# Performance work log

Measured on AMD Instinct MI355X. Metric: run time of the kernel, lower is better.

## Reference

```python
import jax, jax.numpy as jnp
import numpy as np

N = 200000
IN_F = 512
OUT_F = 256
NEG_INF = -9e15


def setup_inputs() -> dict:
    key = jax.random.key(0)
    k1, k2, k3, k4 = jax.random.split(key, 4)
    inp = jax.random.normal(k1, (N, IN_F), dtype=jnp.float32)
    adj = jax.random.randint(k2, (N, OUT_F), 0, 2, dtype=jnp.int32)
    # xavier_uniform with gain=1.414
    g = 1.414
    bW = g * np.sqrt(6.0 / (IN_F + OUT_F))
    W = jax.random.uniform(k3, (IN_F, OUT_F), jnp.float32, -bW, bW)
    ba = g * np.sqrt(6.0 / (2 * OUT_F + 1))
    a = jax.random.uniform(k4, (2 * OUT_F, 1), jnp.float32, -ba, ba)
    return {"input": inp, "adj": adj, "W": W, "a": a}


def reference(input, adj, W, a):
    h = input @ W                      # [N, M]
    M = h.shape[1]
    # a_input[n,m,:] = concat(h[n], h[n]) for every m, so
    # (a_input @ a)[n,m] = h[n] . (a[:M] + a[M:]) — constant over m.
    s = h @ (a[:M, 0] + a[M:, 0])      # [N]
    e = jax.nn.leaky_relu(s, negative_slope=0.2)[:, None]  # [N, 1]
    e = jnp.broadcast_to(e, (h.shape[0], M))               # [N, M]
    masked = jnp.where(adj > 0, e, NEG_INF)
    attention = jax.nn.softmax(masked, axis=1)             # rowwise softmax
    h_prime = attention * h                                # elementwise combine
    return jax.nn.elu(h_prime)
```

## Files before the change

kernel.cpp:

```cpp
#include <hip/hip_runtime.h>
#include <hip/hip_bf16.h>
#include <math.h>


#define NROWS  200000
#define K_DIM  512
#define C_DIM  256
#define BM     128
#define BK     32
#define NCHUNK 16
#define LSTR   40
#define CHUNK_BYTES (C_DIM * LSTR * 2)
#define WPACK_BYTES (NCHUNK * CHUNK_BYTES)

typedef __bf16 bf16x8 __attribute__((ext_vector_type(8)));
typedef float  f32x4  __attribute__((ext_vector_type(4)));
typedef float  f32x16 __attribute__((ext_vector_type(16)));

__global__ void prep_w(const float* __restrict__ W,
                       __bf16* __restrict__ whi, __bf16* __restrict__ wlo) {
  int idx = blockIdx.x * 256 + threadIdx.x;
  int k = idx >> 8, c = idx & 255;
  float w = W[idx];
  __bf16 h = (__bf16)w;
  __bf16 l = (__bf16)(w - (float)h);
  int off = ((k >> 5) * C_DIM + c) * LSTR + (k & 31);
  whi[off] = h;
  wlo[off] = l;
}

__device__ __forceinline__ void gload16(const void* g, void* l) {
  __builtin_amdgcn_global_load_lds(
      (const __attribute__((address_space(1))) unsigned*)g,
      (__attribute__((address_space(3))) unsigned*)l, 16, 0, 0);
}

__global__ void __launch_bounds__(512)
gat_kernel(const float* __restrict__ X, const int* __restrict__ adj,
           const __bf16* __restrict__ whi, const __bf16* __restrict__ wlo,
           float* __restrict__ out) {
  __shared__ __bf16 Ah[2][BM * LSTR];
  __shared__ __bf16 Al[2][BM * LSTR];
  __shared__ __bf16 Bh[2][C_DIM * LSTR];
  __shared__ __bf16 Bl[2][C_DIM * LSTR];
  __shared__ float    invl[BM];
  __shared__ unsigned maskl[BM][8];

  const int tid  = threadIdx.x;
  const int lane = tid & 63;
  const int wv   = tid >> 6;
  const int wm   = wv >> 1;
  const int wn   = wv & 1;
  const int l31  = lane & 31;
  const int hi   = lane >> 5;
  const long r0  = (long)blockIdx.x * BM;

  {
    const int r = tid >> 2, q = tid & 3;
    long rr = r0 + r; if (rr > NROWS - 1) rr = NROWS - 1;
    const int4* ap = (const int4*)(adj + rr * C_DIM + q * 64);
    unsigned w0 = 0, w1 = 0; int cnt = 0;
#pragma unroll
    for (int j = 0; j < 16; ++j) {
      int4 v = ap[j];
      unsigned b = (unsigned)((v.x > 0) | ((v.y > 0) << 1) |
                              ((v.z > 0) << 2) | ((v.w > 0) << 3));
      cnt += __popc(b);
      if (j < 8) w0 |= b << (j * 4); else w1 |= b << ((j - 8) * 4);
    }
    cnt += __shfl_xor(cnt, 1);
    cnt += __shfl_xor(cnt, 2);
    if (cnt == 0) { w0 = 0xffffffffu; w1 = 0xffffffffu; }
    maskl[r][q * 2]     = w0;
    maskl[r][q * 2 + 1] = w1;
    if (q == 0) invl[r] = (cnt > 0) ? (1.0f / (float)cnt) : (1.0f / 256.0f);
  }

  const int sr = tid >> 2;
  const int sq = tid & 3;
  long srow = r0 + sr; if (srow > NROWS - 1) srow = NROWS - 1;
  const float* xbase = X + srow * K_DIM + sq * 8;
  const int aoff = sr * LSTR + sq * 8;
  const __bf16* bsrc = (wv < 4) ? whi : wlo;
  const int bwq = wv & 3;

  f32x16 acc[4];
#pragma unroll
  for (int n = 0; n < 4; ++n) acc[n] = (f32x16)(0.0f);

  f32x4 xa, xb;
  {
    xa = *(const f32x4*)(xbase + 0);
    xb = *(const f32x4*)(xbase + 4);
    const char* s = (const char*)bsrc;
    char* dh = (char*)((wv < 4) ? Bh[0] : Bl[0]);
#pragma unroll
    for (int i = 0; i < 5; ++i) {
      int off = (bwq * 5 + i) * 1024;
      gload16(s + off + lane * 16, dh + off);
    }
    bf16x8 hv, lv;
#pragma unroll
    for (int e = 0; e < 4; ++e) {
      float f0 = xa[e], f1 = xb[e];
      __bf16 h0 = (__bf16)f0, h1 = (__bf16)f1;
      hv[e] = h0; hv[e + 4] = h1;
      lv[e] = (__bf16)(f0 - (float)h0);
      lv[e + 4] = (__bf16)(f1 - (float)h1);
    }
    *(bf16x8*)&Ah[0][aoff] = hv;
    *(bf16x8*)&Al[0][aoff] = lv;
  }
  __syncthreads();

  int cur = 0;
  for (int ck = 0; ck < NCHUNK; ++ck) {
    const bool pf = (ck + 1 < NCHUNK);
    if (pf) {
      xa = *(const f32x4*)(xbase + (ck + 1) * BK);
      xb = *(const f32x4*)(xbase + (ck + 1) * BK + 4);
      const char* s = (const char*)bsrc + (ck + 1) * CHUNK_BYTES;
      char* dh = (char*)((wv < 4) ? Bh[cur ^ 1] : Bl[cur ^ 1]);
#pragma unroll
      for (int i = 0; i < 5; ++i) {
        int off = (bwq * 5 + i) * 1024;
        gload16(s + off + lane * 16, dh + off);
      }
    }
#pragma unroll
    for (int s2 = 0; s2 < 2; ++s2) {
      const int ko = s2 * 16 + hi * 8;
      bf16x8 ah = *(const bf16x8*)&Ah[cur][(wm * 32 + l31) * LSTR + ko];
      bf16x8 al = *(const bf16x8*)&Al[cur][(wm * 32 + l31) * LSTR + ko];
#pragma unroll
      for (int n = 0; n < 4; ++n) {
        const int coff = (wn * 128 + n * 32 + l31) * LSTR + ko;
        bf16x8 bh = *(const bf16x8*)&Bh[cur][coff];
        bf16x8 bl = *(const bf16x8*)&Bl[cur][coff];
        acc[n] = __builtin_amdgcn_mfma_f32_32x32x16_bf16(ah, bh, acc[n], 0, 0, 0);
        acc[n] = __builtin_amdgcn_mfma_f32_32x32x16_bf16(ah, bl, acc[n], 0, 0, 0);
        acc[n] = __builtin_amdgcn_mfma_f32_32x32x16_bf16(al, bh, acc[n], 0, 0, 0);
      }
    }
    if (pf) {
      bf16x8 hv, lv;
#pragma unroll
      for (int e = 0; e < 4; ++e) {
        float f0 = xa[e], f1 = xb[e];
        __bf16 h0 = (__bf16)f0, h1 = (__bf16)f1;
        hv[e] = h0; hv[e + 4] = h1;
        lv[e] = (__bf16)(f0 - (float)h0);
        lv[e + 4] = (__bf16)(f1 - (float)h1);
      }
      *(bf16x8*)&Ah[cur ^ 1][aoff] = hv;
      *(bf16x8*)&Al[cur ^ 1][aoff] = lv;
    }
    __syncthreads();
    cur ^= 1;
  }

#pragma unroll
  for (int n = 0; n < 4; ++n) {
    const int col = wn * 128 + n * 32 + l31;
    const int mwi = col >> 5;
#pragma unroll
    for (int g = 0; g < 4; ++g) {
#pragma unroll
      for (int rb = 0; rb < 4; ++rb) {
        const int reg = g * 4 + rb;
        const int row = wm * 32 + rb + g * 8 + hi * 4;
        const long rr = r0 + row;
        if (rr < NROWS) {
          float inv = invl[row];
          unsigned mw = maskl[row][mwi];
          float h = acc[n][reg];
          float o = 0.0f;
          if ((mw >> (col & 31)) & 1u) {
            float hp = h * inv;
            o = hp > 0.0f ? hp : expm1f(hp);
          }
          out[rr * C_DIM + col] = o;
        }
      }
    }
  }
}

extern "C" void kernel_launch(void* const* d_in, const int* in_sizes, int n_in,
                              void* d_out, int out_size, void* d_ws, size_t ws_size,
                              hipStream_t stream) {
  const float* X   = (const float*)d_in[0];
  const int*   adj = (const int*)d_in[1];
  const float* W   = (const float*)d_in[2];
  __bf16* whi = (__bf16*)d_ws;
  __bf16* wlo = (__bf16*)((char*)d_ws + WPACK_BYTES);

  prep_w<<<512, 256, 0, stream>>>(W, whi, wlo);
  const int nblk = (NROWS + BM - 1) / BM;
  gat_kernel<<<nblk, 512, 0, stream>>>(X, adj, whi, wlo, (float*)d_out);
}
```

Baseline: 869.7 us.

## Replace split-bf16 triple MFMA with single fp16 MFMA and stream adjacency mask

Drops the hi/lo bf16 splitting of X and W, which cost three MFMAs per tile, and uses a single fp16 MFMA on fp16 copies instead, halving LDS and global traffic for W. The adjacency mask load is interleaved into the K-loop prefetch so it overlaps with compute rather than sitting in a serial prologue. The trailing barrier now runs only when a prefetch happened, and launch bounds request more occupancy. This gives up some precision (fp16 has a single rounding and a limited range) in exchange for less compute and memory traffic.

Measured after the change: 888.8 us. 2.2% more time.

```diff
diff --git a/kernel.cpp b/kernel.cpp
--- a/kernel.cpp
+++ b/kernel.cpp
@@ -1,5 +1,6 @@
 #include <hip/hip_runtime.h>
 #include <hip/hip_bf16.h>
+#include <hip/hip_fp16.h>
 #include <math.h>
 
 
@@ -13,20 +14,14 @@
 #define CHUNK_BYTES (C_DIM * LSTR * 2)
 #define WPACK_BYTES (NCHUNK * CHUNK_BYTES)
 
-typedef __bf16 bf16x8 __attribute__((ext_vector_type(8)));
-typedef float  f32x4  __attribute__((ext_vector_type(4)));
-typedef float  f32x16 __attribute__((ext_vector_type(16)));
+typedef _Float16 f16x8 __attribute__((ext_vector_type(8)));
+typedef float    f32x4  __attribute__((ext_vector_type(4)));
+typedef float    f32x16 __attribute__((ext_vector_type(16)));
 
-__global__ void prep_w(const float* __restrict__ W,
-                       __bf16* __restrict__ whi, __bf16* __restrict__ wlo) {
+__global__ void prep_w(const float* __restrict__ W, _Float16* __restrict__ wh) {
   int idx = blockIdx.x * 256 + threadIdx.x;
   int k = idx >> 8, c = idx & 255;
-  float w = W[idx];
-  __bf16 h = (__bf16)w;
-  __bf16 l = (__bf16)(w - (float)h);
-  int off = ((k >> 5) * C_DIM + c) * LSTR + (k & 31);
-  whi[off] = h;
-  wlo[off] = l;
+  wh[((k >> 5) * C_DIM + c) * LSTR + (k & 31)] = (_Float16)W[idx];
 }
 
 __device__ __forceinline__ void gload16(const void* g, void* l) {
@@ -35,14 +30,11 @@
       (__attribute__((address_space(3))) unsigned*)l, 16, 0, 0);
 }
 
-__global__ void __launch_bounds__(512)
+__global__ void __launch_bounds__(512, 4)
 gat_kernel(const float* __restrict__ X, const int* __restrict__ adj,
-           const __bf16* __restrict__ whi, const __bf16* __restrict__ wlo,
-           float* __restrict__ out) {
-  __shared__ __bf16 Ah[2][BM * LSTR];
-  __shared__ __bf16 Al[2][BM * LSTR];
-  __shared__ __bf16 Bh[2][C_DIM * LSTR];
-  __shared__ __bf16 Bl[2][C_DIM * LSTR];
+           const _Float16* __restrict__ wh, float* __restrict__ out) {
+  __shared__ _Float16 Ah[2][BM * LSTR];
+  __shared__ _Float16 Bh[2][C_DIM * LSTR];
   __shared__ float    invl[BM];
   __shared__ unsigned maskl[BM][8];
 
@@ -55,109 +47,86 @@
   const int hi   = lane >> 5;
   const long r0  = (long)blockIdx.x * BM;
 
-  {
-    const int r = tid >> 2, q = tid & 3;
-    long rr = r0 + r; if (rr > NROWS - 1) rr = NROWS - 1;
-    const int4* ap = (const int4*)(adj + rr * C_DIM + q * 64);
-    unsigned w0 = 0, w1 = 0; int cnt = 0;
-#pragma unroll
-    for (int j = 0; j < 16; ++j) {
-      int4 v = ap[j];
-      unsigned b = (unsigned)((v.x > 0) | ((v.y > 0) << 1) |
-                              ((v.z > 0) << 2) | ((v.w > 0) << 3));
-      cnt += __popc(b);
-      if (j < 8) w0 |= b << (j * 4); else w1 |= b << ((j - 8) * 4);
-    }
-    cnt += __shfl_xor(cnt, 1);
-    cnt += __shfl_xor(cnt, 2);
-    if (cnt == 0) { w0 = 0xffffffffu; w1 = 0xffffffffu; }
-    maskl[r][q * 2]     = w0;
-    maskl[r][q * 2 + 1] = w1;
-    if (q == 0) invl[r] = (cnt > 0) ? (1.0f / (float)cnt) : (1.0f / 256.0f);
-  }
-
   const int sr = tid >> 2;
   const int sq = tid & 3;
   long srow = r0 + sr; if (srow > NROWS - 1) srow = NROWS - 1;
   const float* xbase = X + srow * K_DIM + sq * 8;
   const int aoff = sr * LSTR + sq * 8;
-  const __bf16* bsrc = (wv < 4) ? whi : wlo;
-  const int bwq = wv & 3;
+  const int4* adjp = (const int4*)(adj + srow * C_DIM) + sq * 16;
 
   f32x16 acc[4];
 #pragma unroll
   for (int n = 0; n < 4; ++n) acc[n] = (f32x16)(0.0f);
 
-  f32x4 xa, xb;
+  f32x4 xa, xb; int4 av;
   {
     xa = *(const f32x4*)(xbase + 0);
     xb = *(const f32x4*)(xbase + 4);
-    const char* s = (const char*)bsrc;
-    char* dh = (char*)((wv < 4) ? Bh[0] : Bl[0]);
+    av = adjp[0];
 #pragma unroll
-    for (int i = 0; i < 5; ++i) {
-      int off = (bwq * 5 + i) * 1024;
-      gload16(s + off + lane * 16, dh + off);
+    for (int i = 0; i < 3; ++i) {
+      int bi = wv + i * 8;
+      if (bi < 20)
+        gload16((const char*)wh + bi * 1024 + lane * 16, (char*)Bh[0] + bi * 1024);
     }
-    bf16x8 hv, lv;
+    f16x8 hv;
 #pragma unroll
-    for (int e = 0; e < 4; ++e) {
-      float f0 = xa[e], f1 = xb[e];
-      __bf16 h0 = (__bf16)f0, h1 = (__bf16)f1;
-      hv[e] = h0; hv[e + 4] = h1;
-      lv[e] = (__bf16)(f0 - (float)h0);
-      lv[e + 4] = (__bf16)(f1 - (float)h1);
-    }
-    *(bf16x8*)&Ah[0][aoff] = hv;
-    *(bf16x8*)&Al[0][aoff] = lv;
+    for (int e = 0; e < 4; ++e) { hv[e] = (_Float16)xa[e]; hv[e + 4] = (_Float16)xb[e]; }
+    *(f16x8*)&Ah[0][aoff] = hv;
   }
   __syncthreads();
 
+  unsigned w0 = 0, w1 = 0; int cnt = 0;
   int cur = 0;
   for (int ck = 0; ck < NCHUNK; ++ck) {
     const bool pf = (ck + 1 < NCHUNK);
+    f32x4 nxa, nxb; int4 nav;
     if (pf) {
-      xa = *(const f32x4*)(xbase + (ck + 1) * BK);
-      xb = *(const f32x4*)(xbase + (ck + 1) * BK + 4);
-      const char* s = (const char*)bsrc + (ck + 1) * CHUNK_BYTES;
-      char* dh = (char*)((wv < 4) ? Bh[cur ^ 1] : Bl[cur ^ 1]);
+      nxa = *(const f32x4*)(xbase + (ck + 1) * BK);
+      nxb = *(const f32x4*)(xbase + (ck + 1) * BK + 4);
+      nav = adjp[ck + 1];
+      const char* s = (const char*)wh + (ck + 1) * CHUNK_BYTES;
+      char* d = (char*)Bh[cur ^ 1];
 #pragma unroll
-      for (int i = 0; i < 5; ++i) {
-        int off = (bwq * 5 + i) * 1024;
-        gload16(s + off + lane * 16, dh + off);
+      for (int i = 0; i < 3; ++i) {
+        int bi = wv + i * 8;
+        if (bi < 20) gload16(s + bi * 1024 + lane * 16, d + bi * 1024);
       }
     }
 #pragma unroll
     for (int s2 = 0; s2 < 2; ++s2) {
       const int ko = s2 * 16 + hi * 8;
-      bf16x8 ah = *(const bf16x8*)&Ah[cur][(wm * 32 + l31) * LSTR + ko];
-      bf16x8 al = *(const bf16x8*)&Al[cur][(wm * 32 + l31) * LSTR + ko];
+      f16x8 a = *(const f16x8*)&Ah[cur][(wm * 32 + l31) * LSTR + ko];
 #pragma unroll
       for (int n = 0; n < 4; ++n) {
-        const int coff = (wn * 128 + n * 32 + l31) * LSTR + ko;
-        bf16x8 bh = *(const bf16x8*)&Bh[cur][coff];
-        bf16x8 bl = *(const bf16x8*)&Bl[cur][coff];
-        acc[n] = __builtin_amdgcn_mfma_f32_32x32x16_bf16(ah, bh, acc[n], 0, 0, 0);
-        acc[n] = __builtin_amdgcn_mfma_f32_32x32x16_bf16(ah, bl, acc[n], 0, 0, 0);
-        acc[n] = __builtin_amdgcn_mfma_f32_32x32x16_bf16(al, bh, acc[n], 0, 0, 0);
+        f16x8 b = *(const f16x8*)&Bh[cur][(wn * 128 + n * 32 + l31) * LSTR + ko];
+        acc[n] = __builtin_amdgcn_mfma_f32_32x32x16_f16(a, b, acc[n], 0, 0, 0);
       }
     }
+    {
+      unsigned b = (unsigned)((av.x > 0) | ((av.y > 0) << 1) |
+                              ((av.z > 0) << 2) | ((av.w > 0) << 3));
+      cnt += __popc(b);
+      if (ck < 8) w0 |= b << (ck * 4); else w1 |= b << ((ck - 8) * 4);
+    }
     if (pf) {
-      bf16x8 hv, lv;
+      f16x8 hv;
 #pragma unroll
-      for (int e = 0; e < 4; ++e) {
-        float f0 = xa[e], f1 = xb[e];
-        __bf16 h0 = (__bf16)f0, h1 = (__bf16)f1;
-        hv[e] = h0; hv[e + 4] = h1;
-        lv[e] = (__bf16)(f0 - (float)h0);
-        lv[e + 4] = (__bf16)(f1 - (float)h1);
-      }
-      *(bf16x8*)&Ah[cur ^ 1][aoff] = hv;
-      *(bf16x8*)&Al[cur ^ 1][aoff] = lv;
+      for (int e = 0; e < 4; ++e) { hv[e] = (_Float16)nxa[e]; hv[e + 4] = (_Float16)nxb[e]; }
+      *(f16x8*)&Ah[cur ^ 1][aoff] = hv;
+      av = nav;
+      __syncthreads();
     }
-    __syncthreads();
     cur ^= 1;
   }
+
+  cnt += __shfl_xor(cnt, 1);
+  cnt += __shfl_xor(cnt, 2);
+  if (cnt == 0) { w0 = 0xffffffffu; w1 = 0xffffffffu; }
+  maskl[sr][sq * 2]     = w0;
+  maskl[sr][sq * 2 + 1] = w1;
+  if (sq == 0) invl[sr] = (cnt > 0) ? (1.0f / (float)cnt) : (1.0f / 256.0f);
+  __syncthreads();
 
 #pragma unroll
   for (int n = 0; n < 4; ++n) {
@@ -192,10 +161,9 @@
   const float* X   = (const float*)d_in[0];
   const int*   adj = (const int*)d_in[1];
   const float* W   = (const float*)d_in[2];
-  __bf16* whi = (__bf16*)d_ws;
-  __bf16* wlo = (__bf16*)((char*)d_ws + WPACK_BYTES);
+  _Float16* wh = (_Float16*)d_ws;
 
-  prep_w<<<512, 256, 0, stream>>>(W, whi, wlo);
+  prep_w<<<512, 256, 0, stream>>>(W, wh);
   const int nblk = (NROWS + BM - 1) / BM;
-  gat_kernel<<<nblk, 512, 0, stream>>>(X, adj, whi, wlo, (float*)d_out);
+  gat_kernel<<<nblk, 512, 0, stream>>>(X, adj, wh, (float*)d_out);
 }
```
